# Optimization experiments

Hardware: AMD Instinct MI355X
Metric: run time of the kernel (lower is better)

## Reference

```python
import jax, jax.numpy as jnp
import numpy as np

N_NODES = 100000


def _gcn_conv(x, W, b, src, dst, ew, num_nodes):
    # PyG GCNConv: symmetric normalization with self-loops already included
    # in (src, dst, ew). deg computed on destination (col) index.
    deg = jax.ops.segment_sum(ew, dst, num_segments=num_nodes)  # [N]
    dinv = jnp.where(deg > 0, jax.lax.rsqrt(deg), 0.0)          # [N]
    norm = dinv[src] * ew * dinv[dst]                           # [E]
    h = x @ W                                                   # [N, out]
    msg = h[src] * norm[:, None]                                # [E, out] gather+scale
    out = jax.ops.segment_sum(msg, dst, num_segments=num_nodes) # scatter-add
    return out + b


def setup_inputs() -> dict:
    key = jax.random.key(0)
    k = jax.random.split(key, 8)
    in_c, hid_c, out_c = 128, 128, 64
    E, EL = 1600000, 200000
    x = jax.random.normal(k[0], (N_NODES, in_c), dtype=jnp.float32)
    edge_index = jax.random.randint(k[1], (2, E), 0, N_NODES, dtype=jnp.int64)
    edge_weight = jax.random.uniform(k[2], (E,), dtype=jnp.float32)
    edge_label_index = jax.random.randint(k[3], (2, EL), 0, N_NODES, dtype=jnp.int64)
    # Glorot-ish params
    W1 = jax.random.normal(k[4], (in_c, hid_c), dtype=jnp.float32) / np.sqrt(in_c)
    b1 = jnp.zeros((hid_c,), dtype=jnp.float32)
    W2 = jax.random.normal(k[5], (hid_c, out_c), dtype=jnp.float32) / np.sqrt(hid_c)
    b2 = jnp.zeros((out_c,), dtype=jnp.float32)
    return {"x": x, "edge_index": edge_index, "edge_weight": edge_weight,
            "edge_label_index": edge_label_index,
            "W1": W1, "b1": b1, "W2": W2, "b2": b2}


def reference(x, edge_index, edge_weight, edge_label_index, W1, b1, W2, b2):
    n = x.shape[0]
    # add self-loops (weight 1.0), static shape
    loop = jnp.arange(n, dtype=edge_index.dtype)
    src = jnp.concatenate([edge_index[0], loop])
    dst = jnp.concatenate([edge_index[1], loop])
    ew = jnp.concatenate([edge_weight, jnp.ones((n,), dtype=edge_weight.dtype)])
    h = jax.nn.relu(_gcn_conv(x, W1, b1, src, dst, ew, n))
    z = _gcn_conv(h, W2, b2, src, dst, ew, n)          # [N, out_c]
    # decode: edge dot-product
    return (z[edge_label_index[0]] * z[edge_label_index[1]]).sum(axis=-1)
```

## Files before the change

### kernel.cpp

```cpp
#include <hip/hip_runtime.h>
#include <hip/hip_fp16.h>
#include <math.h>

__device__ __forceinline__ float2 h2f2(unsigned int u) {
    __half2 h = *reinterpret_cast<__half2*>(&u);
    return __half22float2(h);
}
__device__ __forceinline__ unsigned int f2h2(float a, float b) {
    __half2 h = __floats2half2_rn(a, b);
    return *reinterpret_cast<unsigned int*>(&h);
}

__global__ __launch_bounds__(256) void gemm128_hist_kernel(
        const float* __restrict__ X, const float* __restrict__ W, __half* __restrict__ Y, int n,
        const int* __restrict__ dst, int* __restrict__ cnt, int* __restrict__ rank, int E) {
    constexpr int CG  = 32;
    constexpr int M   = 64;
    constexpr int RT  = 8;
    constexpr int KC  = 32;
    constexpr int LDX = 132;
    __shared__ float  Xl[M * LDX];
    __shared__ float4 Wl[KC * CG];

    const int bid = blockIdx.x;
    const int t = threadIdx.x;
    const int EPB = (E + (int)gridDim.x - 1) / (int)gridDim.x;
    const int eBeg = bid * EPB;
    const int eEnd = min(eBeg + EPB, E);

    if ((bid & 1) == 0) {
        for (int e = eBeg + t; e < eEnd; e += 256)
            rank[e] = atomicAdd(&cnt[dst[e]], 1);
    }

    int row0 = bid * M;
    {
        const float4* Xg = (const float4*)X;
        for (int f = t; f < M * 32; f += 256) {
            int r = f >> 5, c4 = f & 31;
            int gr = row0 + r;
            float4 v = make_float4(0.f, 0.f, 0.f, 0.f);
            if (gr < n) v = Xg[(size_t)gr * 32 + c4];
            *(float4*)&Xl[r * LDX + c4 * 4] = v;
        }
    }

    int cg = t % CG;
    int r0 = (t / CG) * RT;

    float4 acc[RT];
#pragma unroll
    for (int r = 0; r < RT; r++) acc[r] = make_float4(0.f, 0.f, 0.f, 0.f);

    const float4* Wg = (const float4*)W;
    for (int kc = 0; kc < 128; kc += KC) {
        __syncthreads();
        for (int f = t; f < KC * CG; f += 256)
            Wl[f] = Wg[(size_t)kc * CG + f];
        __syncthreads();
#pragma unroll 4
        for (int k = 0; k < KC; k += 4) {
            float4 b0 = Wl[(k + 0) * CG + cg];
            float4 b1 = Wl[(k + 1) * CG + cg];
            float4 b2 = Wl[(k + 2) * CG + cg];
            float4 b3 = Wl[(k + 3) * CG + cg];
#pragma unroll
            for (int r = 0; r < RT; r++) {
                float4 a = *(float4*)&Xl[(r0 + r) * LDX + kc + k];
                acc[r].x += a.x * b0.x + a.y * b1.x + a.z * b2.x + a.w * b3.x;
                acc[r].y += a.x * b0.y + a.y * b1.y + a.z * b2.y + a.w * b3.y;
                acc[r].z += a.x * b0.z + a.y * b1.z + a.z * b2.z + a.w * b3.z;
                acc[r].w += a.x * b0.w + a.y * b1.w + a.z * b2.w + a.w * b3.w;
            }
        }
    }

#pragma unroll
    for (int r = 0; r < RT; r++) {
        int gr = row0 + r0 + r;
        if (gr < n) {
            uint2 u = make_uint2(f2h2(acc[r].x, acc[r].y), f2h2(acc[r].z, acc[r].w));
            *(uint2*)&Y[(size_t)gr * 128 + cg * 4] = u;
        }
    }

    if (bid & 1) {
        for (int e = eBeg + t; e < eEnd; e += 256)
            rank[e] = atomicAdd(&cnt[dst[e]], 1);
    }
}

__global__ __launch_bounds__(256) void scan_block(const int* __restrict__ in, int* __restrict__ out,
                                                  int* __restrict__ bsum, int n) {
    __shared__ int s[256];
    int tid = threadIdx.x;
    int base = blockIdx.x * 1024 + tid * 4;
    int a0 = (base + 0 < n) ? in[base + 0] : 0;
    int a1 = (base + 1 < n) ? in[base + 1] : 0;
    int a2 = (base + 2 < n) ? in[base + 2] : 0;
    int a3 = (base + 3 < n) ? in[base + 3] : 0;
    int tsum = a0 + a1 + a2 + a3;
    s[tid] = tsum;
    __syncthreads();
    for (int off = 1; off < 256; off <<= 1) {
        int v = (tid >= off) ? s[tid - off] : 0;
        __syncthreads();
        s[tid] += v;
        __syncthreads();
    }
    int texcl = s[tid] - tsum;
    if (base + 0 < n) out[base + 0] = texcl;
    if (base + 1 < n) out[base + 1] = texcl + a0;
    if (base + 2 < n) out[base + 2] = texcl + a0 + a1;
    if (base + 3 < n) out[base + 3] = texcl + a0 + a1 + a2;
    if (tid == 255) bsum[blockIdx.x] = s[255];
}

__global__ __launch_bounds__(256) void scan_bsums(int* __restrict__ bsum, int nb) {
    __shared__ int s[256];
    __shared__ int carry_s;
    int tid = threadIdx.x;
    if (tid == 0) carry_s = 0;
    __syncthreads();
    for (int base = 0; base < nb; base += 256) {
        int v = (base + tid < nb) ? bsum[base + tid] : 0;
        int orig = v;
        s[tid] = v;
        __syncthreads();
        for (int off = 1; off < 256; off <<= 1) {
            int u = (tid >= off) ? s[tid - off] : 0;
            __syncthreads();
            s[tid] += u;
            __syncthreads();
        }
        int carry = carry_s;
        int excl = s[tid] - orig + carry;
        if (base + tid < nb) bsum[base + tid] = excl;
        int tot = s[255];
        __syncthreads();
        if (tid == 0) carry_s = carry + tot;
        __syncthreads();
    }
}

__global__ void scan_add(int* __restrict__ rowptr, const int* __restrict__ bscan, int n) {
    int t = blockIdx.x * blockDim.x + threadIdx.x;
    if (t < n) rowptr[t] += bscan[t >> 10];
}

__global__ void scatter_pairs(const int* __restrict__ src, const int* __restrict__ dst,
                              const float* __restrict__ ew, const int* __restrict__ rowptr,
                              const int* __restrict__ rank, int2* __restrict__ pairs, int E) {
    int e = blockIdx.x * blockDim.x + threadIdx.x;
    if (e >= E) return;
    int d = dst[e];
    int p = rowptr[d] + rank[e];
    pairs[p] = make_int2(src[e], __float_as_int(ew[e]));
}

__global__ void deg_dinv_kernel(const int2* __restrict__ pairs, const int* __restrict__ rowptr,
                                float* __restrict__ dinv, int n) {
    int i = blockIdx.x * blockDim.x + threadIdx.x;
    if (i >= n) return;
    int beg = rowptr[i], end = rowptr[i + 1];
    float s = 0.f;
    for (int j = beg; j < end; j++) s += __int_as_float(pairs[j].y);
    dinv[i] = 1.0f / sqrtf(s + 1.0f);
}

__global__ void premul_kernel(int2* __restrict__ pairs, const float* __restrict__ dinv, int E) {
    int e = blockIdx.x * blockDim.x + threadIdx.x;
    if (e >= E) return;
    int2 p = pairs[e];
    p.y = __float_as_int(__int_as_float(p.y) * dinv[p.x]);
    pairs[e] = p;
}

__global__ __launch_bounds__(512, 8) void gather_mv_kernel(const __half* __restrict__ H,
                                                           const int* __restrict__ rowptr,
                                                           const int2* __restrict__ pairs,
                                                           const float* __restrict__ dinv,
                                                           const float* __restrict__ bias,
                                                           const float* __restrict__ W2,
                                                           __half* __restrict__ Z, int n) {
    __shared__ float h1s[16 * 128];
    __shared__ float w2s[128 * 64];
    const int t = threadIdx.x;
    const int nl = t >> 5;
    const int c4 = t & 31;
    const int node = blockIdx.x * 16 + nl;

    {
        const float4* W2g = (const float4*)W2;
        float4* w2s4 = (float4*)w2s;
#pragma unroll
        for (int f = 0; f < 4; f++) w2s4[f * 512 + t] = W2g[f * 512 + t];
    }

    float4 a0 = make_float4(0.f, 0.f, 0.f, 0.f);
    if (node < n) {
        int beg = rowptr[node], end = rowptr[node + 1];
        float di = dinv[node];
        {
            uint2 hv = *(const uint2*)&H[(size_t)node * 128 + c4 * 4];
            float2 f01 = h2f2(hv.x), f23 = h2f2(hv.y);
            a0.x = f01.x * di; a0.y = f01.y * di; a0.z = f23.x * di; a0.w = f23.y * di;
        }
        float4 a1 = make_float4(0.f, 0.f, 0.f, 0.f);
        float4 a2 = make_float4(0.f, 0.f, 0.f, 0.f);
        float4 a3 = make_float4(0.f, 0.f, 0.f, 0.f);
        int j = beg;
        for (; j + 8 <= end; j += 8) {
            int2 p0 = pairs[j + 0], p1 = pairs[j + 1], p2 = pairs[j + 2], p3 = pairs[j + 3];
            int2 p4 = pairs[j + 4], p5 = pairs[j + 5], p6 = pairs[j + 6], p7 = pairs[j + 7];
            uint2 v0 = *(const uint2*)&H[(size_t)p0.x * 128 + c4 * 4];
            uint2 v1 = *(const uint2*)&H[(size_t)p1.x * 128 + c4 * 4];
            uint2 v2 = *(const uint2*)&H[(size_t)p2.x * 128 + c4 * 4];
            uint2 v3 = *(const uint2*)&H[(size_t)p3.x * 128 + c4 * 4];
            uint2 v4 = *(const uint2*)&H[(size_t)p4.x * 128 + c4 * 4];
            uint2 v5 = *(const uint2*)&H[(size_t)p5.x * 128 + c4 * 4];
            uint2 v6 = *(const uint2*)&H[(size_t)p6.x * 128 + c4 * 4];
            uint2 v7 = *(const uint2*)&H[(size_t)p7.x * 128 + c4 * 4];
            float w0 = __int_as_float(p0.y);
            float w1 = __int_as_float(p1.y);
            float w2 = __int_as_float(p2.y);
            float w3 = __int_as_float(p3.y);
            float w4 = __int_as_float(p4.y);
            float w5 = __int_as_float(p5.y);
            float w6 = __int_as_float(p6.y);
            float w7 = __int_as_float(p7.y);
            float2 f;
            f = h2f2(v0.x); a0.x += f.x * w0; a0.y += f.y * w0;
            f = h2f2(v0.y); a0.z += f.x * w0; a0.w += f.y * w0;
            f = h2f2(v1.x); a1.x += f.x * w1; a1.y += f.y * w1;
            f = h2f2(v1.y); a1.z += f.x * w1; a1.w += f.y * w1;
            f = h2f2(v2.x); a2.x += f.x * w2; a2.y += f.y * w2;
            f = h2f2(v2.y); a2.z += f.x * w2; a2.w += f.y * w2;
            f = h2f2(v3.x); a3.x += f.x * w3; a3.y += f.y * w3;
            f = h2f2(v3.y); a3.z += f.x * w3; a3.w += f.y * w3;
            f = h2f2(v4.x); a0.x += f.x * w4; a0.y += f.y * w4;
            f = h2f2(v4.y); a0.z += f.x * w4; a0.w += f.y * w4;
            f = h2f2(v5.x); a1.x += f.x * w5; a1.y += f.y * w5;
            f = h2f2(v5.y); a1.z += f.x * w5; a1.w += f.y * w5;
            f = h2f2(v6.x); a2.x += f.x * w6; a2.y += f.y * w6;
            f = h2f2(v6.y); a2.z += f.x * w6; a2.w += f.y * w6;
            f = h2f2(v7.x); a3.x += f.x * w7; a3.y += f.y * w7;
            f = h2f2(v7.y); a3.z += f.x * w7; a3.w += f.y * w7;
        }
        for (; j < end; j++) {
            int2 pr = pairs[j];
            float w = __int_as_float(pr.y);
            uint2 v = *(const uint2*)&H[(size_t)pr.x * 128 + c4 * 4];
            float2 f01 = h2f2(v.x), f23 = h2f2(v.y);
            a0.x += f01.x * w; a0.y += f01.y * w; a0.z += f23.x * w; a0.w += f23.y * w;
        }
        float4 bb = ((const float4*)bias)[c4];
        a0.x = fmaxf(((a0.x + a1.x) + (a2.x + a3.x)) * di + bb.x, 0.f);
        a0.y = fmaxf(((a0.y + a1.y) + (a2.y + a3.y)) * di + bb.y, 0.f);
        a0.z = fmaxf(((a0.z + a1.z) + (a2.z + a3.z)) * di + bb.z, 0.f);
        a0.w = fmaxf(((a0.w + a1.w) + (a2.w + a3.w)) * di + bb.w, 0.f);
    }
    *(float4*)&h1s[nl * 128 + c4 * 4] = a0;
    __syncthreads();

    float z0 = 0.f, z1 = 0.f;
    const float* hrow = &h1s[nl * 128];
    const float2* w2c = (const float2*)w2s;
#pragma unroll 8
    for (int k = 0; k < 128; k++) {
        float hk = hrow[k];
        float2 w = w2c[k * 32 + c4];
        z0 += hk * w.x;
        z1 += hk * w.y;
    }
    if (node < n) *(unsigned int*)&Z[(size_t)node * 64 + c4 * 2] = f2h2(z0, z1);
}

__global__ __launch_bounds__(256) void gather_reduce64(const __half* __restrict__ H,
                                                       const int* __restrict__ rowptr,
                                                       const int2* __restrict__ pairs,
                                                       const float* __restrict__ dinv,
                                                       const float* __restrict__ bias,
                                                       __half* __restrict__ out, int n) {
    constexpr int TPN = 16;
    int t = blockIdx.x * blockDim.x + threadIdx.x;
    int node = t / TPN;
    int c4 = t % TPN;
    if (node >= n) return;
    int beg = rowptr[node], end = rowptr[node + 1];
    float di = dinv[node];
    float4 bb = ((const float4*)bias)[c4];
    float4 a0, a1, a2, a3;
    {
        uint2 hv = *(const uint2*)&H[(size_t)node * 64 + c4 * 4];
        float2 f01 = h2f2(hv.x), f23 = h2f2(hv.y);
        a0.x = f01.x * di; a0.y = f01.y * di; a0.z = f23.x * di; a0.w = f23.y * di;
    }
    a1 = make_float4(0.f, 0.f, 0.f, 0.f);
    a2 = make_float4(0.f, 0.f, 0.f, 0.f);
    a3 = make_float4(0.f, 0.f, 0.f, 0.f);
    int j = beg;
    for (; j + 8 <= end; j += 8) {
        int2 p0 = pairs[j + 0], p1 = pairs[j + 1], p2 = pairs[j + 2], p3 = pairs[j + 3];
        int2 p4 = pairs[j + 4], p5 = pairs[j + 5], p6 = pairs[j + 6], p7 = pairs[j + 7];
        uint2 v0 = *(const uint2*)&H[(size_t)p0.x * 64 + c4 * 4];
        uint2 v1 = *(const uint2*)&H[(size_t)p1.x * 64 + c4 * 4];
        uint2 v2 = *(const uint2*)&H[(size_t)p2.x * 64 + c4 * 4];
        uint2 v3 = *(const uint2*)&H[(size_t)p3.x * 64 + c4 * 4];
        uint2 v4 = *(const uint2*)&H[(size_t)p4.x * 64 + c4 * 4];
        uint2 v5 = *(const uint2*)&H[(size_t)p5.x * 64 + c4 * 4];
        uint2 v6 = *(const uint2*)&H[(size_t)p6.x * 64 + c4 * 4];
        uint2 v7 = *(const uint2*)&H[(size_t)p7.x * 64 + c4 * 4];
        float w0 = __int_as_float(p0.y);
        float w1 = __int_as_float(p1.y);
        float w2 = __int_as_float(p2.y);
        float w3 = __int_as_float(p3.y);
        float w4 = __int_as_float(p4.y);
        float w5 = __int_as_float(p5.y);
        float w6 = __int_as_float(p6.y);
        float w7 = __int_as_float(p7.y);
        float2 f;
        f = h2f2(v0.x); a0.x += f.x * w0; a0.y += f.y * w0;
        f = h2f2(v0.y); a0.z += f.x * w0; a0.w += f.y * w0;
        f = h2f2(v1.x); a1.x += f.x * w1; a1.y += f.y * w1;
        f = h2f2(v1.y); a1.z += f.x * w1; a1.w += f.y * w1;
        f = h2f2(v2.x); a2.x += f.x * w2; a2.y += f.y * w2;
        f = h2f2(v2.y); a2.z += f.x * w2; a2.w += f.y * w2;
        f = h2f2(v3.x); a3.x += f.x * w3; a3.y += f.y * w3;
        f = h2f2(v3.y); a3.z += f.x * w3; a3.w += f.y * w3;
        f = h2f2(v4.x); a0.x += f.x * w4; a0.y += f.y * w4;
        f = h2f2(v4.y); a0.z += f.x * w4; a0.w += f.y * w4;
        f = h2f2(v5.x); a1.x += f.x * w5; a1.y += f.y * w5;
        f = h2f2(v5.y); a1.z += f.x * w5; a1.w += f.y * w5;
        f = h2f2(v6.x); a2.x += f.x * w6; a2.y += f.y * w6;
        f = h2f2(v6.y); a2.z += f.x * w6; a2.w += f.y * w6;
        f = h2f2(v7.x); a3.x += f.x * w7; a3.y += f.y * w7;
        f = h2f2(v7.y); a3.z += f.x * w7; a3.w += f.y * w7;
    }
    for (; j < end; j++) {
        int2 pr = pairs[j];
        float w = __int_as_float(pr.y);
        uint2 v = *(const uint2*)&H[(size_t)pr.x * 64 + c4 * 4];
        float2 f01 = h2f2(v.x), f23 = h2f2(v.y);
        a0.x += f01.x * w; a0.y += f01.y * w; a0.z += f23.x * w; a0.w += f23.y * w;
    }
    float4 acc;
    acc.x = ((a0.x + a1.x) + (a2.x + a3.x)) * di + bb.x;
    acc.y = ((a0.y + a1.y) + (a2.y + a3.y)) * di + bb.y;
    acc.z = ((a0.z + a1.z) + (a2.z + a3.z)) * di + bb.z;
    acc.w = ((a0.w + a1.w) + (a2.w + a3.w)) * di + bb.w;
    uint2 u = make_uint2(f2h2(acc.x, acc.y), f2h2(acc.z, acc.w));
    *(uint2*)&out[(size_t)node * 64 + c4 * 4] = u;
}

__global__ void decode_kernel(const __half* __restrict__ Z, const int* __restrict__ ea,
                              const int* __restrict__ eb, float* __restrict__ out, int L) {
    int t = blockIdx.x * blockDim.x + threadIdx.x;
    int e = t >> 4;
    int c = (t & 15) << 2;
    if (e >= L) return;
    uint2 ua = *(const uint2*)&Z[(size_t)ea[e] * 64 + c];
    uint2 ub = *(const uint2*)&Z[(size_t)eb[e] * 64 + c];
    float2 a01 = h2f2(ua.x), a23 = h2f2(ua.y);
    float2 b01 = h2f2(ub.x), b23 = h2f2(ub.y);
    float p = a01.x * b01.x + a01.y * b01.y + a23.x * b23.x + a23.y * b23.y;
    p += __shfl_xor(p, 1);
    p += __shfl_xor(p, 2);
    p += __shfl_xor(p, 4);
    p += __shfl_xor(p, 8);
    if ((t & 15) == 0) out[e] = p;
}

extern "C" void kernel_launch(void* const* d_in, const int* in_sizes, int n_in,
                              void* d_out, int out_size, void* d_ws, size_t ws_size,
                              hipStream_t stream) {
    const float* x   = (const float*)d_in[0];
    const int*   ei  = (const int*)d_in[1];
    const float* ew  = (const float*)d_in[2];
    const int*   eli = (const int*)d_in[3];
    const float* W1  = (const float*)d_in[4];
    const float* b1  = (const float*)d_in[5];
    const float* W2  = (const float*)d_in[6];
    const float* b2  = (const float*)d_in[7];
    float* out = (float*)d_out;

    const int N = in_sizes[0] / 128;
    const int E = in_sizes[2];
    const int L = in_sizes[3] / 2;
    const int NP = ((N + 255) / 256) * 256;

    float* ws     = (float*)d_ws;
    float* dinv   = ws;
    int*   cnt    = (int*)(ws + NP);
    int*   rowptr = cnt + NP;
    int*   bsum   = rowptr + NP;
    int*   rank   = bsum + 1024;
    int2*  pairs  = (int2*)(rank + E);
    __half* A     = (__half*)(pairs + E);
    __half* B     = (__half*)((float*)(pairs + E) + (size_t)NP * 128);
    __half* Zf    = A;

    const int n1 = N + 1;
    const int nb = (n1 + 1023) / 1024;

    hipMemsetAsync(cnt, 0, (size_t)n1 * 4, stream);

    const int Gg = (N + 63) / 64;
    gemm128_hist_kernel<<<Gg, 256, 0, stream>>>(x, W1, A, N, ei + E, cnt, rank, E);

    scan_block<<<nb, 256, 0, stream>>>(cnt, rowptr, bsum, n1);
    scan_bsums<<<1, 256, 0, stream>>>(bsum, nb);
    scan_add<<<(n1 + 255) / 256, 256, 0, stream>>>(rowptr, bsum, n1);
    scatter_pairs<<<(E + 255) / 256, 256, 0, stream>>>(ei, ei + E, ew, rowptr, rank, pairs, E);
    deg_dinv_kernel<<<(N + 255) / 256, 256, 0, stream>>>(pairs, rowptr, dinv, N);
    premul_kernel<<<(E + 255) / 256, 256, 0, stream>>>(pairs, dinv, E);

    gather_mv_kernel<<<(N + 15) / 16, 512, 0, stream>>>(A, rowptr, pairs, dinv, b1, W2, B, N);

    gather_reduce64<<<(N * 16 + 255) / 256, 256, 0, stream>>>(B, rowptr, pairs, dinv, b2, Zf, N);

    decode_kernel<<<(L * 16 + 255) / 256, 256, 0, stream>>>(Zf, eli, eli + L, out, L);
}
```

Before: 434.1 us.

## Compute degree via atomics in histogram pass, fold premul into scatter, prefetch pairs

Edge weights are now accumulated per destination with float atomics during the histogram pass. A small kernel computes dinv from those sums, and scatter_pairs writes the pre-multiplied weight directly. This removes the separate deg_dinv and premul passes over the pairs array. Both gather kernels are rewritten with a software-pipelined loop that prefetches the next 8 pairs while gathering the current ones, handling tails by masking. Launch bounds are also changed. The cost is extra atomic traffic in the histogram pass and float-atomic nondeterminism in the degree sums.

```diff
diff --git a/kernel.cpp b/kernel.cpp
--- a/kernel.cpp
+++ b/kernel.cpp
@@ -13,7 +13,8 @@
 
 __global__ __launch_bounds__(256) void gemm128_hist_kernel(
         const float* __restrict__ X, const float* __restrict__ W, __half* __restrict__ Y, int n,
-        const int* __restrict__ dst, int* __restrict__ cnt, int* __restrict__ rank, int E) {
+        const int* __restrict__ dst, const float* __restrict__ ew,
+        int* __restrict__ cnt, float* __restrict__ wsum, int* __restrict__ rank, int E) {
     constexpr int CG  = 32;
     constexpr int M   = 64;
     constexpr int RT  = 8;
@@ -29,8 +30,11 @@
     const int eEnd = min(eBeg + EPB, E);
 
     if ((bid & 1) == 0) {
-        for (int e = eBeg + t; e < eEnd; e += 256)
-            rank[e] = atomicAdd(&cnt[dst[e]], 1);
+        for (int e = eBeg + t; e < eEnd; e += 256) {
+            int d = dst[e];
+            rank[e] = atomicAdd(&cnt[d], 1);
+            atomicAdd(&wsum[d], ew[e]);
+        }
     }
 
     int row0 = bid * M;
@@ -85,8 +89,11 @@
     }
 
     if (bid & 1) {
-        for (int e = eBeg + t; e < eEnd; e += 256)
-            rank[e] = atomicAdd(&cnt[dst[e]], 1);
+        for (int e = eBeg + t; e < eEnd; e += 256) {
+            int d = dst[e];
+            rank[e] = atomicAdd(&cnt[d], 1);
+            atomicAdd(&wsum[d], ew[e]);
+        }
     }
 }
 
@@ -148,35 +155,25 @@
     if (t < n) rowptr[t] += bscan[t >> 10];
 }
 
+__global__ void dinv_kernel(const float* __restrict__ wsum, float* __restrict__ dinv, int n) {
+    int i = blockIdx.x * blockDim.x + threadIdx.x;
+    if (i >= n) return;
+    dinv[i] = 1.0f / sqrtf(wsum[i] + 1.0f);
+}
+
 __global__ void scatter_pairs(const int* __restrict__ src, const int* __restrict__ dst,
                               const float* __restrict__ ew, const int* __restrict__ rowptr,
-                              const int* __restrict__ rank, int2* __restrict__ pairs, int E) {
+                              const int* __restrict__ rank, const float* __restrict__ dinv,
+                              int2* __restrict__ pairs, int E) {
     int e = blockIdx.x * blockDim.x + threadIdx.x;
     if (e >= E) return;
     int d = dst[e];
+    int s = src[e];
     int p = rowptr[d] + rank[e];
-    pairs[p] = make_int2(src[e], __float_as_int(ew[e]));
-}
-
-__global__ void deg_dinv_kernel(const int2* __restrict__ pairs, const int* __restrict__ rowptr,
-                                float* __restrict__ dinv, int n) {
-    int i = blockIdx.x * blockDim.x + threadIdx.x;
-    if (i >= n) return;
-    int beg = rowptr[i], end = rowptr[i + 1];
-    float s = 0.f;
-    for (int j = beg; j < end; j++) s += __int_as_float(pairs[j].y);
-    dinv[i] = 1.0f / sqrtf(s + 1.0f);
-}
-
-__global__ void premul_kernel(int2* __restrict__ pairs, const float* __restrict__ dinv, int E) {
-    int e = blockIdx.x * blockDim.x + threadIdx.x;
-    if (e >= E) return;
-    int2 p = pairs[e];
-    p.y = __float_as_int(__int_as_float(p.y) * dinv[p.x]);
-    pairs[e] = p;
-}
-
-__global__ __launch_bounds__(512, 8) void gather_mv_kernel(const __half* __restrict__ H,
+    pairs[p] = make_int2(s, __float_as_int(ew[e] * dinv[s]));
+}
+
+__global__ __launch_bounds__(512, 4) void gather_mv_kernel(const __half* __restrict__ H,
                                                            const int* __restrict__ rowptr,
                                                            const int2* __restrict__ pairs,
                                                            const float* __restrict__ dinv,
@@ -197,68 +194,59 @@
         for (int f = 0; f < 4; f++) w2s4[f * 512 + t] = W2g[f * 512 + t];
     }
 
+    float4 acc[4];
+#pragma unroll
+    for (int i = 0; i < 4; i++) acc[i] = make_float4(0.f, 0.f, 0.f, 0.f);
+
+    float di = 0.f;
+    int beg = 0, end = 0;
+    if (node < n) {
+        beg = rowptr[node]; end = rowptr[node + 1];
+        di = dinv[node];
+        uint2 hv = *(const uint2*)&H[(size_t)node * 128 + c4 * 4];
+        float2 f01 = h2f2(hv.x), f23 = h2f2(hv.y);
+        acc[0].x = f01.x * di; acc[0].y = f01.y * di;
+        acc[0].z = f23.x * di; acc[0].w = f23.y * di;
+    }
+
+    if (beg < end) {
+        int2 pc[8];
+#pragma unroll
+        for (int i = 0; i < 8; i++) {
+            int jj = beg + i;
+            pc[i] = pairs[jj < end ? jj : beg];
+        }
+        for (int j = beg; j < end; j += 8) {
+            uint2 v[8];
+#pragma unroll
+            for (int i = 0; i < 8; i++)
+                v[i] = *(const uint2*)&H[(size_t)(unsigned)pc[i].x * 128 + c4 * 4];
+            int2 pn[8];
+            int jn = j + 8;
+#pragma unroll
+            for (int i = 0; i < 8; i++) {
+                int jj = jn + i;
+                pn[i] = pairs[jj < end ? jj : beg];
+            }
+#pragma unroll
+            for (int i = 0; i < 8; i++) {
+                float w = (j + i < end) ? __int_as_float(pc[i].y) : 0.f;
+                float2 g01 = h2f2(v[i].x), g23 = h2f2(v[i].y);
+                acc[i & 3].x += g01.x * w; acc[i & 3].y += g01.y * w;
+                acc[i & 3].z += g23.x * w; acc[i & 3].w += g23.y * w;
+            }
+#pragma unroll
+            for (int i = 0; i < 8; i++) pc[i] = pn[i];
+        }
+    }
+
     float4 a0 = make_float4(0.f, 0.f, 0.f, 0.f);
     if (node < n) {
-        int beg = rowptr[node], end = rowptr[node + 1];
-        float di = dinv[node];
-        {
-            uint2 hv = *(const uint2*)&H[(size_t)node * 128 + c4 * 4];
-            float2 f01 = h2f2(hv.x), f23 = h2f2(hv.y);
-            a0.x = f01.x * di; a0.y = f01.y * di; a0.z = f23.x * di; a0.w = f23.y * di;
-        }
-        float4 a1 = make_float4(0.f, 0.f, 0.f, 0.f);
-        float4 a2 = make_float4(0.f, 0.f, 0.f, 0.f);
-        float4 a3 = make_float4(0.f, 0.f, 0.f, 0.f);
-        int j = beg;
-        for (; j + 8 <= end; j += 8) {
-            int2 p0 = pairs[j + 0], p1 = pairs[j + 1], p2 = pairs[j + 2], p3 = pairs[j + 3];
-            int2 p4 = pairs[j + 4], p5 = pairs[j + 5], p6 = pairs[j + 6], p7 = pairs[j + 7];
-            uint2 v0 = *(const uint2*)&H[(size_t)p0.x * 128 + c4 * 4];
-            uint2 v1 = *(const uint2*)&H[(size_t)p1.x * 128 + c4 * 4];
-            uint2 v2 = *(const uint2*)&H[(size_t)p2.x * 128 + c4 * 4];
-            uint2 v3 = *(const uint2*)&H[(size_t)p3.x * 128 + c4 * 4];
-            uint2 v4 = *(const uint2*)&H[(size_t)p4.x * 128 + c4 * 4];
-            uint2 v5 = *(const uint2*)&H[(size_t)p5.x * 128 + c4 * 4];
-            uint2 v6 = *(const uint2*)&H[(size_t)p6.x * 128 + c4 * 4];
-            uint2 v7 = *(const uint2*)&H[(size_t)p7.x * 128 + c4 * 4];
-            float w0 = __int_as_float(p0.y);
-            float w1 = __int_as_float(p1.y);
-            float w2 = __int_as_float(p2.y);
-            float w3 = __int_as_float(p3.y);
-            float w4 = __int_as_float(p4.y);
-            float w5 = __int_as_float(p5.y);
-            float w6 = __int_as_float(p6.y);
-            float w7 = __int_as_float(p7.y);
-            float2 f;
-            f = h2f2(v0.x); a0.x += f.x * w0; a0.y += f.y * w0;
-            f = h2f2(v0.y); a0.z += f.x * w0; a0.w += f.y * w0;
-            f = h2f2(v1.x); a1.x += f.x * w1; a1.y += f.y * w1;
-            f = h2f2(v1.y); a1.z += f.x * w1; a1.w += f.y * w1;
-            f = h2f2(v2.x); a2.x += f.x * w2; a2.y += f.y * w2;
-            f = h2f2(v2.y); a2.z += f.x * w2; a2.w += f.y * w2;
-            f = h2f2(v3.x); a3.x += f.x * w3; a3.y += f.y * w3;
-            f = h2f2(v3.y); a3.z += f.x * w3; a3.w += f.y * w3;
-            f = h2f2(v4.x); a0.x += f.x * w4; a0.y += f.y * w4;
-            f = h2f2(v4.y); a0.z += f.x * w4; a0.w += f.y * w4;
-            f = h2f2(v5.x); a1.x += f.x * w5; a1.y += f.y * w5;
-            f = h2f2(v5.y); a1.z += f.x * w5; a1.w += f.y * w5;
-            f = h2f2(v6.x); a2.x += f.x * w6; a2.y += f.y * w6;
-            f = h2f2(v6.y); a2.z += f.x * w6; a2.w += f.y * w6;
-            f = h2f2(v7.x); a3.x += f.x * w7; a3.y += f.y * w7;
-            f = h2f2(v7.y); a3.z += f.x * w7; a3.w += f.y * w7;
-        }
-        for (; j < end; j++) {
-            int2 pr = pairs[j];
-            float w = __int_as_float(pr.y);
-            uint2 v = *(const uint2*)&H[(size_t)pr.x * 128 + c4 * 4];
-            float2 f01 = h2f2(v.x), f23 = h2f2(v.y);
-            a0.x += f01.x * w; a0.y += f01.y * w; a0.z += f23.x * w; a0.w += f23.y * w;
-        }
         float4 bb = ((const float4*)bias)[c4];
-        a0.x = fmaxf(((a0.x + a1.x) + (a2.x + a3.x)) * di + bb.x, 0.f);
-        a0.y = fmaxf(((a0.y + a1.y) + (a2.y + a3.y)) * di + bb.y, 0.f);
-        a0.z = fmaxf(((a0.z + a1.z) + (a2.z + a3.z)) * di + bb.z, 0.f);
-        a0.w = fmaxf(((a0.w + a1.w) + (a2.w + a3.w)) * di + bb.w, 0.f);
+        a0.x = fmaxf(((acc[0].x + acc[1].x) + (acc[2].x + acc[3].x)) * di + bb.x, 0.f);
+        a0.y = fmaxf(((acc[0].y + acc[1].y) + (acc[2].y + acc[3].y)) * di + bb.y, 0.f);
+        a0.z = fmaxf(((acc[0].z + acc[1].z) + (acc[2].z + acc[3].z)) * di + bb.z, 0.f);
+        a0.w = fmaxf(((acc[0].w + acc[1].w) + (acc[2].w + acc[3].w)) * di + bb.w, 0.f);
     }
     *(float4*)&h1s[nl * 128 + c4 * 4] = a0;
     __syncthreads();
@@ -276,12 +264,12 @@
     if (node < n) *(unsigned int*)&Z[(size_t)node * 64 + c4 * 2] = f2h2(z0, z1);
 }
 
-__global__ __launch_bounds__(256) void gather_reduce64(const __half* __restrict__ H,
-                                                       const int* __restrict__ rowptr,
-                                                       const int2* __restrict__ pairs,
-                                                       const float* __restrict__ dinv,
-                                                       const float* __restrict__ bias,
-                                                       __half* __restrict__ out, int n) {
+__global__ __launch_bounds__(256, 4) void gather_reduce64(const __half* __restrict__ H,
+                                                          const int* __restrict__ rowptr,
+                                                          const int2* __restrict__ pairs,
+                                                          const float* __restrict__ dinv,
+                                                          const float* __restrict__ bias,
+                                                          __half* __restrict__ out, int n) {
     constexpr int TPN = 16;
     int t = blockIdx.x * blockDim.x + threadIdx.x;
     int node = t / TPN;
@@ -290,66 +278,53 @@
     int beg = rowptr[node], end = rowptr[node + 1];
     float di = dinv[node];
     float4 bb = ((const float4*)bias)[c4];
-    float4 a0, a1, a2, a3;
+    float4 acc[4];
     {
         uint2 hv = *(const uint2*)&H[(size_t)node * 64 + c4 * 4];
         float2 f01 = h2f2(hv.x), f23 = h2f2(hv.y);
-        a0.x = f01.x * di; a0.y = f01.y * di; a0.z = f23.x * di; a0.w = f23.y * di;
-    }
-    a1 = make_float4(0.f, 0.f, 0.f, 0.f);
-    a2 = make_float4(0.f, 0.f, 0.f, 0.f);
-    a3 = make_float4(0.f, 0.f, 0.f, 0.f);
-    int j = beg;
-    for (; j + 8 <= end; j += 8) {
-        int2 p0 = pairs[j + 0], p1 = pairs[j + 1], p2 = pairs[j + 2], p3 = pairs[j + 3];
-        int2 p4 = pairs[j + 4], p5 = pairs[j + 5], p6 = pairs[j + 6], p7 = pairs[j + 7];
-        uint2 v0 = *(const uint2*)&H[(size_t)p0.x * 64 + c4 * 4];
-        uint2 v1 = *(const uint2*)&H[(size_t)p1.x * 64 + c4 * 4];
-        uint2 v2 = *(const uint2*)&H[(size_t)p2.x * 64 + c4 * 4];
-        uint2 v3 = *(const uint2*)&H[(size_t)p3.x * 64 + c4 * 4];
-        uint2 v4 = *(const uint2*)&H[(size_t)p4.x * 64 + c4 * 4];
-        uint2 v5 = *(const uint2*)&H[(size_t)p5.x * 64 + c4 * 4];
-        uint2 v6 = *(const uint2*)&H[(size_t)p6.x * 64 + c4 * 4];
-        uint2 v7 = *(const uint2*)&H[(size_t)p7.x * 64 + c4 * 4];
-        float w0 = __int_as_float(p0.y);
-        float w1 = __int_as_float(p1.y);
-        float w2 = __int_as_float(p2.y);
-        float w3 = __int_as_float(p3.y);
-        float w4 = __int_as_float(p4.y);
-        float w5 = __int_as_float(p5.y);
-        float w6 = __int_as_float(p6.y);
-        float w7 = __int_as_float(p7.y);
-        float2 f;
-        f = h2f2(v0.x); a0.x += f.x * w0; a0.y += f.y * w0;
-        f = h2f2(v0.y); a0.z += f.x * w0; a0.w += f.y * w0;
-        f = h2f2(v1.x); a1.x += f.x * w1; a1.y += f.y * w1;
-        f = h2f2(v1.y); a1.z += f.x * w1; a1.w += f.y * w1;
-        f = h2f2(v2.x); a2.x += f.x * w2; a2.y += f.y * w2;
-        f = h2f2(v2.y); a2.z += f.x * w2; a2.w += f.y * w2;
-        f = h2f2(v3.x); a3.x += f.x * w3; a3.y += f.y * w3;
-        f = h2f2(v3.y); a3.z += f.x * w3; a3.w += f.y * w3;
-        f = h2f2(v4.x); a0.x += f.x * w4; a0.y += f.y * w4;
-        f = h2f2(v4.y); a0.z += f.x * w4; a0.w += f.y * w4;
-        f = h2f2(v5.x); a1.x += f.x * w5; a1.y += f.y * w5;
-        f = h2f2(v5.y); a1.z += f.x * w5; a1.w += f.y * w5;
-        f = h2f2(v6.x); a2.x += f.x * w6; a2.y += f.y * w6;
-        f = h2f2(v6.y); a2.z += f.x * w6; a2.w += f.y * w6;
-        f = h2f2(v7.x); a3.x += f.x * w7; a3.y += f.y * w7;
-        f = h2f2(v7.y); a3.z += f.x * w7; a3.w += f.y * w7;
-    }
-    for (; j < end; j++) {
-        int2 pr = pairs[j];
-        float w = __int_as_float(pr.y);
-        uint2 v = *(const uint2*)&H[(size_t)pr.x * 64 + c4 * 4];
-        float2 f01 = h2f2(v.x), f23 = h2f2(v.y);
-        a0.x += f01.x * w; a0.y += f01.y * w; a0.z += f23.x * w; a0.w += f23.y * w;
-    }
-    float4 acc;
-    acc.x = ((a0.x + a1.x) + (a2.x + a3.x)) * di + bb.x;
-    acc.y = ((a0.y + a1.y) + (a2.y + a3.y)) * di + bb.y;
-    acc.z = ((a0.z + a1.z) + (a2.z + a3.z)) * di + bb.z;
-    acc.w = ((a0.w + a1.w) + (a2.w + a3.w)) * di + bb.w;
-    uint2 u = make_uint2(f2h2(acc.x, acc.y), f2h2(acc.z, acc.w));
+        acc[0].x = f01.x * di; acc[0].y = f01.y * di;
+        acc[0].z = f23.x * di; acc[0].w = f23.y * di;
+    }
+#pragma unroll
+    for (int i = 1; i < 4; i++) acc[i] = make_float4(0.f, 0.f, 0.f, 0.f);
+
+    if (beg < end) {
+        int2 pc[8];
+#pragma unroll
+        for (int i = 0; i < 8; i++) {
+            int jj = beg + i;
+            pc[i] = pairs[jj < end ? jj : beg];
+        }
+        for (int j = beg; j < end; j += 8) {
+            uint2 v[8];
+#pragma unroll
+            for (int i = 0; i < 8; i++)
+                v[i] = *(const uint2*)&H[(size_t)(unsigned)pc[i].x * 64 + c4 * 4];
+            int2 pn[8];
+            int jn = j + 8;
+#pragma unroll
+            for (int i = 0; i < 8; i++) {
+                int jj = jn + i;
+                pn[i] = pairs[jj < end ? jj : beg];
+            }
+#pragma unroll
+            for (int i = 0; i < 8; i++) {
+                float w = (j + i < end) ? __int_as_float(pc[i].y) : 0.f;
+                float2 g01 = h2f2(v[i].x), g23 = h2f2(v[i].y);
+                acc[i & 3].x += g01.x * w; acc[i & 3].y += g01.y * w;
+                acc[i & 3].z += g23.x * w; acc[i & 3].w += g23.y * w;
+            }
+#pragma unroll
+            for (int i = 0; i < 8; i++) pc[i] = pn[i];
+        }
+    }
+
+    float4 r;
+    r.x = ((acc[0].x + acc[1].x) + (acc[2].x + acc[3].x)) * di + bb.x;
+    r.y = ((acc[0].y + acc[1].y) + (acc[2].y + acc[3].y)) * di + bb.y;
+    r.z = ((acc[0].z + acc[1].z) + (acc[2].z + acc[3].z)) * di + bb.z;
+    r.w = ((acc[0].w + acc[1].w) + (acc[2].w + acc[3].w)) * di + bb.w;
+    uint2 u = make_uint2(f2h2(r.x, r.y), f2h2(r.z, r.w));
     *(uint2*)&out[(size_t)node * 64 + c4 * 4] = u;
 }
 
@@ -391,7 +366,8 @@
 
     float* ws     = (float*)d_ws;
     float* dinv   = ws;
-    int*   cnt    = (int*)(ws + NP);
+    float* wsum   = ws + NP;
+    int*   cnt    = (int*)(wsum + NP);
     int*   rowptr = cnt + NP;
     int*   bsum   = rowptr + NP;
     int*   rank   = bsum + 1024;
@@ -403,17 +379,17 @@
     const int n1 = N + 1;
     const int nb = (n1 + 1023) / 1024;
 
-    hipMemsetAsync(cnt, 0, (size_t)n1 * 4, stream);
+    hipMemsetAsync(wsum, 0, ((size_t)NP + (size_t)n1) * 4, stream);
 
     const int Gg = (N + 63) / 64;
-    gemm128_hist_kernel<<<Gg, 256, 0, stream>>>(x, W1, A, N, ei + E, cnt, rank, E);
+    gemm128_hist_kernel<<<Gg, 256, 0, stream>>>(x, W1, A, N, ei + E, ew, cnt, wsum, rank, E);
+
+    dinv_kernel<<<(N + 255) / 256, 256, 0, stream>>>(wsum, dinv, N);
 
     scan_block<<<nb, 256, 0, stream>>>(cnt, rowptr, bsum, n1);
     scan_bsums<<<1, 256, 0, stream>>>(bsum, nb);
     scan_add<<<(n1 + 255) / 256, 256, 0, stream>>>(rowptr, bsum, n1);
-    scatter_pairs<<<(E + 255) / 256, 256, 0, stream>>>(ei, ei + E, ew, rowptr, rank, pairs, E);
-    deg_dinv_kernel<<<(N + 255) / 256, 256, 0, stream>>>(pairs, rowptr, dinv, N);
-    premul_kernel<<<(E + 255) / 256, 256, 0, stream>>>(pairs, dinv, E);
+    scatter_pairs<<<(E + 255) / 256, 256, 0, stream>>>(ei, ei + E, ew, rowptr, rank, dinv, pairs, E);
 
     gather_mv_kernel<<<(N + 15) / 16, 512, 0, stream>>>(A, rowptr, pairs, dinv, b1, W2, B, N);
 
```

After: 471.1 us. 8.5% more time.
